# Kernel optimization log

Measured on AMD Instinct MI355X. Metric: run time of the kernel, lower is better.

The kernel has to match this reference:

```python
import jax, jax.numpy as jnp
import numpy as np

B, K, N = 8192, 4096, 4096
GROUP = 128
G = K // GROUP
NLEVELS = 16


def setup_inputs() -> dict:
    key = jax.random.key(0)
    k1, k2, k3, k4, k5 = jax.random.split(key, 5)
    x = jax.random.normal(k1, (B, K), dtype=jnp.float32)
    indices = jax.random.randint(k2, (N, K), 0, NLEVELS, dtype=jnp.int32)
    codebook = jax.random.normal(k3, (NLEVELS,), dtype=jnp.float32)
    weight_norms = jax.random.uniform(k4, (N, G), dtype=jnp.float32)
    # per-group orthogonal rotation matrices (QR of Gaussian, as in rotation='qr')
    A = jax.random.normal(k5, (G, GROUP, GROUP), dtype=jnp.float32)
    Q, _ = jnp.linalg.qr(A)  # (G, GROUP, GROUP)
    return {"x": x, "indices": indices, "codebook": codebook,
            "weight_norms": weight_norms, "rotations": Q}


def reference(x, indices, codebook, weight_norms, rotations):
    """TurboQuantLinear forward (single pass, no bias, no residual).

    For each group g:
      x_rot_g = x[:, gs:ge] @ Pi_g.T
      out    += (x_rot_g @ codebook[idx_g].T) * (norms[:, g] / sqrt(group_size))
    Vectorized over groups.
    """
    b, k = x.shape
    g, gs, _ = rotations.shape
    n = indices.shape[0]
    scale = jnp.sqrt(jnp.asarray(gs, dtype=x.dtype))
    xg = x.reshape(b, g, gs)                                   # (B, G, gs)
    x_rot = jnp.einsum('bgk,gjk->bgj', xg, rotations)          # x_g @ Pi_g.T
    W = codebook[indices].reshape(n, g, gs)                    # dequant (N, G, gs)
    out = jnp.einsum('bgj,ngj,ng->bn', x_rot, W, weight_norms) / scale
    return out
```

## Files before the change

### kernel.cpp

```cpp
#include <hip/hip_runtime.h>
#include <hip/hip_bf16.h>

#define B_DIM 8192
#define K_DIM 4096
#define N_DIM 4096
#define GROUP 128
#define NG    (K_DIM / GROUP)
#define INV_SQRT_GROUP 0.08838834764831845f

using bf16x8 = __attribute__((ext_vector_type(8))) short;
using f32x4  = __attribute__((ext_vector_type(4))) float;

__device__ inline unsigned short f2bf(float f) {
    union { float f; unsigned u; } v; v.f = f;
    unsigned r = v.u + 0x7fffu + ((v.u >> 16) & 1u);
    return (unsigned short)(r >> 16);
}

#define GLOAD_LDS16(gp, lp)                                                   \
    __builtin_amdgcn_global_load_lds(                                         \
        (__attribute__((address_space(1))) void*)(gp),                        \
        (__attribute__((address_space(3))) void*)(lp), 16, 0, 0)

#define BAR()                                                                 \
    {                                                                         \
        asm volatile("" ::: "memory");                                        \
        __builtin_amdgcn_s_barrier();                                         \
        asm volatile("" ::: "memory");                                        \
    }
#define LGKM0()  asm volatile("s_waitcnt lgkmcnt(0)" ::: "memory")
#define VMCNT(n) asm volatile("s_waitcnt vmcnt(" #n ")" ::: "memory")
#define PRIO(p)  __builtin_amdgcn_s_setprio(p)

__global__ __launch_bounds__(256) void cast_x_kernel(
    const float* __restrict__ x, unsigned short* __restrict__ xb, size_t n8)
{
    size_t i = (size_t)blockIdx.x * blockDim.x + threadIdx.x;
    if (i >= n8) return;
    const float4* xp = (const float4*)x;
    float4 a = xp[2 * i];
    float4 b = xp[2 * i + 1];
    union { unsigned short s[8]; uint4 v; } pk;
    pk.s[0] = f2bf(a.x); pk.s[1] = f2bf(a.y); pk.s[2] = f2bf(a.z); pk.s[3] = f2bf(a.w);
    pk.s[4] = f2bf(b.x); pk.s[5] = f2bf(b.y); pk.s[6] = f2bf(b.z); pk.s[7] = f2bf(b.w);
    ((uint4*)xb)[i] = pk.v;
}

__global__ __launch_bounds__(256) void cast_rot_kernel(
    const float* __restrict__ rot, unsigned short* __restrict__ Rt)
{
    const int g = blockIdx.x;
    const float* Rg = rot + (size_t)g * GROUP * GROUP;
    unsigned short* Rtg = Rt + (size_t)g * GROUP * GROUP;
    for (int e = threadIdx.x; e < 128 * 32; e += 256) {
        int j = e >> 5, kc = (e & 31) * 4;
        float4 v = *(const float4*)(Rg + (size_t)j * 128 + kc);
        Rtg[(size_t)(kc + 0) * 128 + j] = f2bf(v.x);
        Rtg[(size_t)(kc + 1) * 128 + j] = f2bf(v.y);
        Rtg[(size_t)(kc + 2) * 128 + j] = f2bf(v.z);
        Rtg[(size_t)(kc + 3) * 128 + j] = f2bf(v.w);
    }
}

__global__ __launch_bounds__(256) void prep_v_kernel(
    const int*   __restrict__ indices,
    const float* __restrict__ codebook,
    const float* __restrict__ norms,
    const unsigned short* __restrict__ Rt,
    unsigned short* __restrict__ Vout)
{
    const int g  = blockIdx.y;
    const int n0 = blockIdx.x * 128;
    const int tid = threadIdx.x;

    __shared__ __attribute__((aligned(16))) unsigned short w_lds[128][136];
    __shared__ float s_lds[128];
    __shared__ float cb_lds[16];

    if (tid < 16)  cb_lds[tid] = codebook[tid];
    if (tid < 128) s_lds[tid] = norms[(size_t)(n0 + tid) * NG + g] * INV_SQRT_GROUP;
    __syncthreads();

    for (int e = tid; e < 128 * 16; e += 256) {
        const int nl = e >> 4, jc = e & 15;
        const float s = s_lds[nl];
        const int4* ip = (const int4*)(indices + (size_t)(n0 + nl) * K_DIM + g * GROUP + jc * 8);
        int4 i0 = ip[0];
        int4 i1 = ip[1];
        union { unsigned short h[8]; uint4 v; } pk;
        pk.h[0] = f2bf(cb_lds[i0.x] * s); pk.h[1] = f2bf(cb_lds[i0.y] * s);
        pk.h[2] = f2bf(cb_lds[i0.z] * s); pk.h[3] = f2bf(cb_lds[i0.w] * s);
        pk.h[4] = f2bf(cb_lds[i1.x] * s); pk.h[5] = f2bf(cb_lds[i1.y] * s);
        pk.h[6] = f2bf(cb_lds[i1.z] * s); pk.h[7] = f2bf(cb_lds[i1.w] * s);
        *(uint4*)&w_lds[nl][jc * 8] = pk.v;
    }
    __syncthreads();

    const int lane = tid & 63;
    const int wv   = tid >> 6;
    const int l15  = lane & 15;
    const int quad = lane >> 4;
    const int wn = (wv >> 1) * 64;
    const int wk = (wv & 1) * 64;

    const unsigned short* Rtg = Rt + (size_t)g * GROUP * GROUP;

    f32x4 acc[4][4] = {};

    for (int js = 0; js < 4; ++js) {
        const int jo = js * 32 + quad * 8;
        bf16x8 aF[4], bF[4];
        for (int mi = 0; mi < 4; ++mi)
            aF[mi] = *(const bf16x8*)&w_lds[wn + mi * 16 + l15][jo];
        for (int ni = 0; ni < 4; ++ni) {
            const int k = wk + ni * 16 + l15;
            bF[ni] = *(const bf16x8*)(Rtg + (size_t)k * 128 + jo);
        }
        for (int mi = 0; mi < 4; ++mi)
            for (int ni = 0; ni < 4; ++ni)
                acc[mi][ni] = __builtin_amdgcn_mfma_f32_16x16x32_bf16(
                    aF[mi], bF[ni], acc[mi][ni], 0, 0, 0);
    }

    for (int mi = 0; mi < 4; ++mi) {
        int n = n0 + wn + mi * 16 + quad * 4;
        for (int ni = 0; ni < 4; ++ni) {
            int k = wk + ni * 16 + l15;
            unsigned short* dst = Vout + (size_t)n * K_DIM + g * GROUP + k;
            for (int r = 0; r < 4; ++r)
                dst[(size_t)r * K_DIM] = f2bf(acc[mi][ni][r]);
        }
    }
}

template <int GRP, int NLO>
__device__ __forceinline__ void mfma_quad(f32x4 (&acc)[8][4],
                                          const bf16x8 (&aF)[4][2],
                                          const bf16x8 (&bF)[4][2])
{
#pragma unroll
    for (int mi = 0; mi < 4; ++mi)
#pragma unroll
        for (int nn = 0; nn < 2; ++nn)
#pragma unroll
            for (int kh = 0; kh < 2; ++kh)
                acc[GRP * 4 + mi][NLO + nn] = __builtin_amdgcn_mfma_f32_16x16x32_bf16(
                    aF[mi][kh], bF[NLO + nn][kh], acc[GRP * 4 + mi][NLO + nn], 0, 0, 0);
}

__global__ __launch_bounds__(512) void gemm256_kernel(
    const unsigned short* __restrict__ A,
    const unsigned short* __restrict__ Bm,
    float* __restrict__ C)
{
    const int tid = threadIdx.x;
    const int n0 = blockIdx.x * 256;
    const int m0 = blockIdx.y * 256;

    __shared__ __attribute__((aligned(16))) unsigned short a_lds[2 * 256 * 64];
    __shared__ __attribute__((aligned(16))) unsigned short b_lds[2 * 256 * 64];

    const int lane = tid & 63;
    const int wv   = tid >> 6;
    const int l15  = lane & 15;
    const int quad = lane >> 4;
    const int wm   = wv >> 2;
    const int wn   = wv & 3;

    int rr[4], ko[4], lb[4];
#pragma unroll
    for (int p = 0; p < 4; ++p) {
        int c = tid + 512 * p;
        rr[p] = c >> 3;
        ko[p] = ((c & 7) ^ ((c >> 3) & 7)) * 8;
        lb[p] = (tid & ~63) + 512 * p;
    }

    const int koh0 = ((0 * 4 + quad) ^ (l15 & 7)) * 8;
    const int koh1 = ((1 * 4 + quad) ^ (l15 & 7)) * 8;
    const int aBase = (wm * 128 + l15) * 64;
    const int bBase = (wn * 64 + l15) * 64;

    f32x4 acc[8][4] = {};
    bf16x8 aF[4][2], bF[4][2];

#define STAGE_A(bb, kt, p)                                                    \
    GLOAD_LDS16(A + (size_t)(m0 + rr[p]) * K_DIM + (size_t)(kt) * 64 + ko[p], \
                a_lds + (bb) * 16384 + lb[p] * 8)
#define STAGE_B(bb, kt, p)                                                    \
    GLOAD_LDS16(Bm + (size_t)(n0 + rr[p]) * K_DIM + (size_t)(kt) * 64 + ko[p],\
                b_lds + (bb) * 16384 + lb[p] * 8)

#pragma unroll
    for (int p = 0; p < 4; ++p) STAGE_A(0, 0, p);
#pragma unroll
    for (int p = 0; p < 4; ++p) STAGE_B(0, 0, p);
#pragma unroll
    for (int p = 0; p < 4; ++p) STAGE_A(1, 1, p);
    VMCNT(4);
    BAR();

    for (int t = 0; t < 64; ++t) {
        const int b = t & 1;
        const int boff = b * 16384;

#pragma unroll
        for (int mi = 0; mi < 4; ++mi) {
            aF[mi][0] = *(const bf16x8*)&a_lds[boff + aBase + mi * 1024 + koh0];
            aF[mi][1] = *(const bf16x8*)&a_lds[boff + aBase + mi * 1024 + koh1];
        }
#pragma unroll
        for (int nn = 0; nn < 2; ++nn) {
            bF[nn][0] = *(const bf16x8*)&b_lds[boff + bBase + nn * 1024 + koh0];
            bF[nn][1] = *(const bf16x8*)&b_lds[boff + bBase + nn * 1024 + koh1];
        }
        if (t + 1 < 64) { STAGE_B(b ^ 1, t + 1, 0); STAGE_B(b ^ 1, t + 1, 1); }
        BAR(); LGKM0();
        PRIO(1); mfma_quad<0, 0>(acc, aF, bF); PRIO(0);
        BAR();

#pragma unroll
        for (int nn = 2; nn < 4; ++nn) {
            bF[nn][0] = *(const bf16x8*)&b_lds[boff + bBase + nn * 1024 + koh0];
            bF[nn][1] = *(const bf16x8*)&b_lds[boff + bBase + nn * 1024 + koh1];
        }
        if (t + 1 < 64) { STAGE_B(b ^ 1, t + 1, 2); STAGE_B(b ^ 1, t + 1, 3); }
        BAR(); LGKM0();
        PRIO(1); mfma_quad<0, 2>(acc, aF, bF); PRIO(0);
        BAR();

#pragma unroll
        for (int mi = 0; mi < 4; ++mi) {
            aF[mi][0] = *(const bf16x8*)&a_lds[boff + aBase + 4096 + mi * 1024 + koh0];
            aF[mi][1] = *(const bf16x8*)&a_lds[boff + aBase + 4096 + mi * 1024 + koh1];
        }
        BAR(); LGKM0();
        PRIO(1); mfma_quad<1, 0>(acc, aF, bF); PRIO(0);
        BAR();

        if (t + 2 < 64) {
#pragma unroll
            for (int p = 0; p < 4; ++p) STAGE_A(b, t + 2, p);
        }
        BAR();
        PRIO(1); mfma_quad<1, 2>(acc, aF, bF); PRIO(0);
        if (t < 62)       { VMCNT(4); }
        else if (t == 62) { VMCNT(0); }
        BAR();
    }

#pragma unroll
    for (int mi = 0; mi < 8; ++mi) {
        int m = m0 + wm * 128 + mi * 16 + quad * 4;
#pragma unroll
        for (int ni = 0; ni < 4; ++ni) {
            int n = n0 + wn * 64 + ni * 16 + l15;
            float* dst = C + (size_t)m * N_DIM + n;
#pragma unroll
            for (int r = 0; r < 4; ++r)
                dst[(size_t)r * N_DIM] = acc[mi][ni][r];
        }
    }
#undef STAGE_A
#undef STAGE_B
}

extern "C" void kernel_launch(void* const* d_in, const int* in_sizes, int n_in,
                              void* d_out, int out_size, void* d_ws, size_t ws_size,
                              hipStream_t stream)
{
    const float* x        = (const float*)d_in[0];
    const int*   indices  = (const int*)d_in[1];
    const float* codebook = (const float*)d_in[2];
    const float* norms    = (const float*)d_in[3];
    const float* rot      = (const float*)d_in[4];
    float* out            = (float*)d_out;

    unsigned short* Rt = (unsigned short*)d_ws;
    unsigned short* Xb = Rt + (size_t)NG * GROUP * GROUP;
    unsigned short* V  = Xb + (size_t)B_DIM * K_DIM;

    {
        size_t n8 = (size_t)B_DIM * K_DIM / 8;
        cast_x_kernel<<<dim3((unsigned)(n8 / 256)), dim3(256), 0, stream>>>(x, Xb, n8);
        cast_rot_kernel<<<dim3(NG), dim3(256), 0, stream>>>(rot, Rt);
    }
    {
        dim3 grid(N_DIM / 128, NG);
        prep_v_kernel<<<grid, dim3(256), 0, stream>>>(indices, codebook, norms, Rt, V);
    }
    {
        dim3 grid(N_DIM / 256, B_DIM / 256);
        gemm256_kernel<<<grid, dim3(512), 0, stream>>>(Xb, V, out);
    }
}
```

Before: 543.5 us.

## Deepen B prefetch to two tiles ahead, swizzle block order, coalesce weight stores

Result: slower. 583.3 us (+7.3%).

```diff
diff --git a/kernel.cpp b/kernel.cpp
--- a/kernel.cpp
+++ b/kernel.cpp
@@ -122,13 +122,25 @@
                     aF[mi], bF[ni], acc[mi][ni], 0, 0, 0);
     }
 
+    __syncthreads();
+
     for (int mi = 0; mi < 4; ++mi) {
-        int n = n0 + wn + mi * 16 + quad * 4;
+        const int nl = wn + mi * 16 + quad * 4;
         for (int ni = 0; ni < 4; ++ni) {
-            int k = wk + ni * 16 + l15;
-            unsigned short* dst = Vout + (size_t)n * K_DIM + g * GROUP + k;
+            const int kl = wk + ni * 16 + l15;
             for (int r = 0; r < 4; ++r)
-                dst[(size_t)r * K_DIM] = f2bf(acc[mi][ni][r]);
+                w_lds[nl + r][kl] = f2bf(acc[mi][ni][r]);
+        }
+    }
+    __syncthreads();
+
+    {
+        const int rlo = tid >> 4;
+        const int col = (tid & 15) * 8;
+        for (int pass = 0; pass < 8; ++pass) {
+            const int row = pass * 16 + rlo;
+            uint4 v = *(const uint4*)&w_lds[row][col];
+            *(uint4*)(Vout + (size_t)(n0 + row) * K_DIM + g * GROUP + col) = v;
         }
     }
 }
@@ -154,8 +166,11 @@
     float* __restrict__ C)
 {
     const int tid = threadIdx.x;
-    const int n0 = blockIdx.x * 256;
-    const int m0 = blockIdx.y * 256;
+
+    const int flat = blockIdx.y * gridDim.x + blockIdx.x;
+    const int swz  = (flat & 7) * 64 + (flat >> 3);
+    const int n0 = (swz & 15) * 256;
+    const int m0 = (swz >> 4) * 256;
 
     __shared__ __attribute__((aligned(16))) unsigned short a_lds[2 * 256 * 64];
     __shared__ __attribute__((aligned(16))) unsigned short b_lds[2 * 256 * 64];
@@ -197,7 +212,9 @@
     for (int p = 0; p < 4; ++p) STAGE_B(0, 0, p);
 #pragma unroll
     for (int p = 0; p < 4; ++p) STAGE_A(1, 1, p);
-    VMCNT(4);
+#pragma unroll
+    for (int p = 0; p < 4; ++p) STAGE_B(1, 1, p);
+    VMCNT(8);
     BAR();
 
     for (int t = 0; t < 64; ++t) {
@@ -214,7 +231,6 @@
             bF[nn][0] = *(const bf16x8*)&b_lds[boff + bBase + nn * 1024 + koh0];
             bF[nn][1] = *(const bf16x8*)&b_lds[boff + bBase + nn * 1024 + koh1];
         }
-        if (t + 1 < 64) { STAGE_B(b ^ 1, t + 1, 0); STAGE_B(b ^ 1, t + 1, 1); }
         BAR(); LGKM0();
         PRIO(1); mfma_quad<0, 0>(acc, aF, bF); PRIO(0);
         BAR();
@@ -224,7 +240,6 @@
             bF[nn][0] = *(const bf16x8*)&b_lds[boff + bBase + nn * 1024 + koh0];
             bF[nn][1] = *(const bf16x8*)&b_lds[boff + bBase + nn * 1024 + koh1];
         }
-        if (t + 1 < 64) { STAGE_B(b ^ 1, t + 1, 2); STAGE_B(b ^ 1, t + 1, 3); }
         BAR(); LGKM0();
         PRIO(1); mfma_quad<0, 2>(acc, aF, bF); PRIO(0);
         BAR();
@@ -234,17 +249,19 @@
             aF[mi][0] = *(const bf16x8*)&a_lds[boff + aBase + 4096 + mi * 1024 + koh0];
             aF[mi][1] = *(const bf16x8*)&a_lds[boff + aBase + 4096 + mi * 1024 + koh1];
         }
+        if (t + 2 < 64) { STAGE_B(b, t + 2, 0); STAGE_B(b, t + 2, 1); }
         BAR(); LGKM0();
         PRIO(1); mfma_quad<1, 0>(acc, aF, bF); PRIO(0);
         BAR();
 
         if (t + 2 < 64) {
+            STAGE_B(b, t + 2, 2); STAGE_B(b, t + 2, 3);
 #pragma unroll
             for (int p = 0; p < 4; ++p) STAGE_A(b, t + 2, p);
         }
         BAR();
         PRIO(1); mfma_quad<1, 2>(acc, aF, bF); PRIO(0);
-        if (t < 62)       { VMCNT(4); }
+        if (t < 62)       { VMCNT(8); }
         else if (t == 62) { VMCNT(0); }
         BAR();
     }
```
